# Optimization experiments

Hardware: AMD Instinct MI355X
Metric: run time of the kernel (lower is better)

Reference implementation:

```python
import jax, jax.numpy as jnp
import numpy as np

N_NODES = 100000
N_EDGES = 1600000
IN_F = 67
H1, C1 = 10, 8   # heads, per-head channels layer 1
H2, C2 = 1, 1    # layer 2


def setup_inputs() -> dict:
    key = jax.random.key(0)
    ks = jax.random.split(key, 10)
    x = jax.random.normal(ks[0], (N_NODES, IN_F), dtype=jnp.float32)
    edge_index = jax.random.randint(ks[1], (2, N_EDGES), 0, N_NODES, dtype=jnp.int64)
    s = 0.1
    W1 = jax.random.normal(ks[2], (IN_F, H1 * C1), dtype=jnp.float32) * s
    att_src1 = jax.random.normal(ks[3], (H1, C1), dtype=jnp.float32) * s
    att_dst1 = jax.random.normal(ks[4], (H1, C1), dtype=jnp.float32) * s
    b1 = jnp.zeros((H1 * C1,), dtype=jnp.float32)
    W2 = jax.random.normal(ks[5], (H1 * C1, H2 * C2), dtype=jnp.float32) * s
    att_src2 = jax.random.normal(ks[6], (H2, C2), dtype=jnp.float32) * s
    att_dst2 = jax.random.normal(ks[7], (H2, C2), dtype=jnp.float32) * s
    b2 = jnp.zeros((H2 * C2,), dtype=jnp.float32)
    return {"x": x, "edge_index": edge_index, "W1": W1, "att_src1": att_src1,
            "att_dst1": att_dst1, "b1": b1, "W2": W2, "att_src2": att_src2,
            "att_dst2": att_dst2, "b2": b2}


def gat_conv(x, src, dst, W, att_src, att_dst, bias, heads, out_ch):
    """PyG GATConv (eval mode): gather -> leaky_relu -> segment softmax -> scatter."""
    n = x.shape[0]
    h = (x @ W).reshape(n, heads, out_ch)                     # [N,H,C]
    a_src = jnp.sum(h * att_src, axis=-1)                     # [N,H]
    a_dst = jnp.sum(h * att_dst, axis=-1)                     # [N,H]
    e = a_src[src] + a_dst[dst]                               # [E,H]
    e = jax.nn.leaky_relu(e, negative_slope=0.2)
    # numerically stable softmax over edges grouped by destination node
    m = jax.ops.segment_max(e, dst, num_segments=n)           # [N,H]
    ex = jnp.exp(e - m[dst])
    denom = jax.ops.segment_sum(ex, dst, num_segments=n)      # [N,H]
    alpha = ex / denom[dst]                                   # [E,H]
    msg = h[src] * alpha[:, :, None]                          # [E,H,C]
    out = jax.ops.segment_sum(msg, dst, num_segments=n)       # [N,H,C]
    return out.reshape(n, heads * out_ch) + bias


def reference(x, edge_index, W1, att_src1, att_dst1, b1, W2, att_src2, att_dst2, b2):
    n = x.shape[0]
    loops = jnp.arange(n, dtype=edge_index.dtype)
    src = jnp.concatenate([edge_index[0], loops])             # add_self_loops=True
    dst = jnp.concatenate([edge_index[1], loops])
    h = gat_conv(x, src, dst, W1, att_src1, att_dst1, b1, H1, C1)
    h = jax.nn.elu(h)
    out = gat_conv(h, src, dst, W2, att_src2, att_dst2, b2, H2, C2)
    return out
```

## Files before the change

### kernel.cpp

```cpp
#include <hip/hip_runtime.h>
#include <math.h>

#define IN_F 67
#define F1   80
#define NH1  10
#define NC1  8

#define GN   64
#define KS   104
#define PKS  96

#define CB    512
#define CSH   9
#define NBC   196
#define RB    64
#define NGRP  8
#define GCAP  1536
#define SLCAP 1664
#define CSTRIDE 16
#define NFB   782
#define CHUNK 2048
#define A2T   4

typedef _Float16 h16;
typedef h16 h16x2 __attribute__((ext_vector_type(2)));
typedef h16 h16x8 __attribute__((ext_vector_type(8)));
typedef float f32x4 __attribute__((ext_vector_type(4)));
typedef float f32x4u __attribute__((ext_vector_type(4), aligned(4)));
typedef int i32x4 __attribute__((ext_vector_type(4)));

__global__ __launch_bounds__(256)
void k_front(const float* __restrict__ x, const float* __restrict__ W,
             const float* __restrict__ att_s, const float* __restrict__ att_d,
             const int* __restrict__ ei, int* __restrict__ gcur,
             int* __restrict__ ebuf, h16* __restrict__ pk,
             float* __restrict__ a_dst, int N, int E) {
    __shared__ __align__(16) char smem[GN * 81 * 4];
    const int tid = threadIdx.x;

    if ((int)blockIdx.x < NFB) {
        int2* sStage = (int2*)smem;
        int*  sCnt   = (int*)(smem + CHUNK * 8);
        int*  sGBase = sCnt + NBC;
        int*  sScan  = sGBase + NBC;
        int*  wsum   = sScan + 256;
        const int g = blockIdx.x & (NGRP - 1);
        const int lane = tid & 63;
        const int wv = tid >> 6;

        int base_e = blockIdx.x * CHUNK;
        if (base_e < E) {
            int lim = E - base_e; if (lim > CHUNK) lim = CHUNK;
            for (int i = tid; i < NBC; i += 256) sCnt[i] = 0;
            __syncthreads();

            int2 ev[8]; int pos[8]; int nloc = 0;
            int e0 = base_e + tid * 8;
            if (tid * 8 + 8 <= lim) {
                i32x4 s0 = *(const i32x4*)(ei + e0);
                i32x4 s1 = *(const i32x4*)(ei + e0 + 4);
                i32x4 d0 = *(const i32x4*)(ei + E + e0);
                i32x4 d1 = *(const i32x4*)(ei + E + e0 + 4);
#pragma unroll
                for (int j = 0; j < 4; ++j) { ev[j] = make_int2(s0[j], d0[j]); }
#pragma unroll
                for (int j = 0; j < 4; ++j) { ev[4 + j] = make_int2(s1[j], d1[j]); }
                nloc = 8;
            } else {
                for (int j = 0; j < 8; ++j) {
                    int e = e0 + j;
                    if (tid * 8 + j < lim) { ev[nloc++] = make_int2(ei[e], ei[E + e]); }
                }
            }
            for (int j = 0; j < nloc; ++j)
                pos[j] = atomicAdd(&sCnt[ev[j].y >> CSH], 1);
            __syncthreads();

            int v = (tid < NBC) ? sCnt[tid] : 0;
            int sc = v;
#pragma unroll
            for (int o = 1; o < 64; o <<= 1) {
                int u = __shfl_up(sc, o);
                if (lane >= o) sc += u;
            }
            if (lane == 63) wsum[wv] = sc;
            __syncthreads();
            int add = 0;
#pragma unroll
            for (int w = 0; w < 4; ++w) add += (w < wv) ? wsum[w] : 0;
            sScan[tid] = sc + add;
            if (tid < NBC && v > 0)
                sGBase[tid] = atomicAdd(&gcur[((size_t)g * NBC + tid) * CSTRIDE], v);
            __syncthreads();

            for (int j = 0; j < nloc; ++j) {
                int B = ev[j].y >> CSH;
                sStage[sScan[B] - sCnt[B] + pos[j]] = ev[j];
            }
            __syncthreads();

            int total = sScan[NBC - 1];
            for (int i = tid; i < total; i += 256) {
                int2 e = sStage[i];
                int B = e.y >> CSH;
                int gp = sGBase[B] + (i - (sScan[B] - sCnt[B]));
                if (gp < GCAP)
                    ebuf[((size_t)g * NBC + B) * GCAP + gp] = e.x | ((e.y & (CB - 1)) << 17);
            }
        }
        return;
    }

    h16*   sWt = (h16*)smem;
    float* sO  = (float*)smem;
    const int node0 = (blockIdx.x - NFB) * GN;

    for (int idx = tid; idx < F1 * 96; idx += 256) {
        int k = idx / F1;
        int c = idx - k * F1;
        sWt[c * KS + k] = (h16)(k < IN_F ? W[idx] : 0.f);
    }
    __syncthreads();

    const int lane = tid & 63;
    const int m    = lane & 15;
    const int quad = lane >> 4;
    const int wn0  = (tid >> 6) * 16;

    int gn  = node0 + wn0 + m;
    int gnc = gn < N ? gn : N - 1;
    const float* xr = x + (size_t)gnc * IN_F;

    f32x4 acc[5];
#pragma unroll
    for (int ct = 0; ct < 5; ++ct) acc[ct] = (f32x4){0.f, 0.f, 0.f, 0.f};

#pragma unroll
    for (int ks = 0; ks < 64; ks += 32) {
        int k0 = ks + quad * 8;
        f32x4 a0 = *(const f32x4u*)(xr + k0);
        f32x4 a1 = *(const f32x4u*)(xr + k0 + 4);
        h16x8 af;
        af[0] = (h16)a0.x; af[1] = (h16)a0.y; af[2] = (h16)a0.z; af[3] = (h16)a0.w;
        af[4] = (h16)a1.x; af[5] = (h16)a1.y; af[6] = (h16)a1.z; af[7] = (h16)a1.w;
#pragma unroll
        for (int ct = 0; ct < 5; ++ct) {
            h16x8 bf = *(const h16x8*)(sWt + (ct * 16 + m) * KS + ks + quad * 8);
            acc[ct] = __builtin_amdgcn_mfma_f32_16x16x32_f16(af, bf, acc[ct], 0, 0, 0);
        }
    }
    {
        h16x8 af = (h16x8)(h16)0.f;
        if (quad == 0) {
            af[0] = (h16)xr[64]; af[1] = (h16)xr[65]; af[2] = (h16)xr[66];
        }
#pragma unroll
        for (int ct = 0; ct < 5; ++ct) {
            h16x8 bf = *(const h16x8*)(sWt + (ct * 16 + m) * KS + 64 + quad * 8);
            acc[ct] = __builtin_amdgcn_mfma_f32_16x16x32_f16(af, bf, acc[ct], 0, 0, 0);
        }
    }
    __syncthreads();

#pragma unroll
    for (int ct = 0; ct < 5; ++ct)
#pragma unroll
        for (int r = 0; r < 4; ++r)
            sO[(wn0 + quad * 4 + r) * 81 + ct * 16 + m] = acc[ct][r];
    __syncthreads();

    for (int idx = tid; idx < GN * (F1 / 2); idx += 256) {
        int n = idx / (F1 / 2);
        int p = idx - n * (F1 / 2);
        int gg = node0 + n;
        if (gg < N) {
            h16x2 v;
            v.x = (h16)sO[n * 81 + 2 * p];
            v.y = (h16)sO[n * 81 + 2 * p + 1];
            *(h16x2*)(pk + (size_t)gg * PKS + 2 * p) = v;
        }
    }
    for (int t = tid; t < GN * NH1; t += 256) {
        int n = t / NH1;
        int h = t - n * NH1;
        int gg = node0 + n;
        if (gg < N) {
            const float* hr = sO + n * 81 + h * NC1;
            float s = 0.f, d = 0.f;
#pragma unroll
            for (int c = 0; c < NC1; ++c) {
                float v = hr[c];
                s += v * att_s[h * NC1 + c];
                d += v * att_d[h * NC1 + c];
            }
            pk[(size_t)gg * PKS + F1 + h] = (h16)s;
            a_dst[gg * NH1 + h] = d;
        }
    }
}

__global__ __launch_bounds__(256)
void k_agg1(const int* __restrict__ ebuf, const int* __restrict__ gcur,
            const h16* __restrict__ pk, const float* __restrict__ a_dst,
            const float* __restrict__ b1, const float* __restrict__ W2,
            float* __restrict__ hl2acc,
            int* __restrict__ row, int* __restrict__ deg, int* __restrict__ csr2,
            int N, int NB) {
    __shared__ int   sTmp[SLCAP];
    __shared__ int   sList[SLCAP];
    __shared__ int   s_cnt[RB];
    __shared__ int   s_scan[RB];
    __shared__ int   s_cur[RB];
    __shared__ float s_acc[RB];
    __shared__ int   sTot;

    const int tid = threadIdx.x;
    const int lane = tid & 63;
    const int b = blockIdx.x;
    const int B = b >> 3;
    const int q = b & 7;
    const int lo = b * RB;

    for (int i = tid; i < RB; i += 256) { s_cnt[i] = 1; s_acc[i] = 0.f; }
    if (tid == 0) sTot = 0;
    __syncthreads();

    for (int g = 0; g < NGRP; ++g) {
        size_t slot = (size_t)g * NBC + B;
        int cnt = gcur[slot * CSTRIDE];
        cnt = cnt < GCAP ? cnt : GCAP;
        const int* eb = ebuf + slot * GCAP;
        for (int i0 = 0; i0 < cnt; i0 += 256) {
            int i = i0 + tid;
            int v = 0, n_l = 0;
            bool match = false;
            if (i < cnt) {
                v = eb[i];
                int dloc = v >> 17;
                match = (dloc >> 6) == q;
                n_l = dloc & (RB - 1);
            }
            unsigned long long mk = __ballot(match);
            int base = 0;
            if (lane == 0 && mk) base = atomicAdd(&sTot, __popcll(mk));
            base = __shfl(base, 0);
            if (match) {
                atomicAdd(&s_cnt[n_l], 1);
                int p = base + __popcll(mk & ((1ull << lane) - 1));
                if (p < SLCAP) sTmp[p] = (v & 0x1FFFF) | (n_l << 17);
            }
        }
    }
    __syncthreads();

    if (tid < RB) {
        int cntv = s_cnt[tid];
        int sc = cntv;
#pragma unroll
        for (int o = 1; o < RB; o <<= 1) {
            int u = __shfl_up(sc, o);
            if (tid >= o) sc += u;
        }
        s_scan[tid] = sc;
        int excl = sc - cntv;
        int n = lo + tid;
        if (excl < SLCAP) sList[excl] = n;
        s_cur[tid] = excl + 1;
        if (n < N) {
            int dg = cntv;
            if (excl + dg > SLCAP) dg = SLCAP - excl > 0 ? SLCAP - excl : 0;
            row[n] = b * SLCAP + excl;
            deg[n] = dg;
        }
    }
    __syncthreads();

    int total = sTot < SLCAP ? sTot : SLCAP;
    for (int i = tid; i < total; i += 256) {
        int u = sTmp[i];
        int n_l = u >> 17;
        int p = atomicAdd(&s_cur[n_l], 1);
        if (p < SLCAP) sList[p] = u & 0x1FFFF;
    }
    __syncthreads();

    int tot2 = s_scan[RB - 1];
    tot2 = tot2 < SLCAP ? tot2 : SLCAP;
    for (int i = tid; i < tot2; i += 256)
        csr2[(size_t)b * SLCAP + i] = sList[i];

    for (int t = tid; t < RB * NH1; t += 256) {
        int n_l = t / NH1;
        int h = t - n_l * NH1;
        int n = lo + n_l;
        if (n >= N) continue;
        int beg = s_scan[n_l] - s_cnt[n_l];
        int end = beg + s_cnt[n_l];
        end = end < SLCAP ? end : SLCAP;
        float ad = a_dst[n * NH1 + h];
        float den = 0.f;
        float num[NC1];
#pragma unroll
        for (int c = 0; c < NC1; ++c) num[c] = 0.f;

        int i = beg;
        for (; i + 3 < end; i += 4) {
            int sv[4];
#pragma unroll
            for (int j = 0; j < 4; ++j) sv[j] = sList[i + j];
            h16x8 qf[4];
            float a[4];
#pragma unroll
            for (int j = 0; j < 4; ++j) {
                const h16* rp = pk + (size_t)sv[j] * PKS;
                qf[j] = *(const h16x8*)(rp + h * NC1);
                a[j] = (float)rp[F1 + h];
            }
#pragma unroll
            for (int j = 0; j < 4; ++j) {
                float v = a[j] + ad;
                v = v > 0.f ? v : 0.2f * v;
                float w = __expf(v);
                den += w;
#pragma unroll
                for (int c = 0; c < NC1; ++c) num[c] += w * (float)qf[j][c];
            }
        }
        for (; i < end; ++i) {
            const h16* rp = pk + (size_t)sList[i] * PKS;
            h16x8 qf = *(const h16x8*)(rp + h * NC1);
            float v = (float)rp[F1 + h] + ad;
            v = v > 0.f ? v : 0.2f * v;
            float w = __expf(v);
            den += w;
#pragma unroll
            for (int c = 0; c < NC1; ++c) num[c] += w * (float)qf[c];
        }
        float inv = 1.f / den;
        const float* bb = b1 + h * NC1;
        const float* w2 = W2 + h * NC1;
        float p = 0.f;
#pragma unroll
        for (int c = 0; c < NC1; ++c) {
            float o = num[c] * inv + bb[c];
            o = o > 0.f ? o : expm1f(o);
            p += o * w2[c];
        }
        atomicAdd(&s_acc[n_l], p);
    }
    __syncthreads();

    if (tid < RB) {
        int n = lo + tid;
        if (n < N) hl2acc[n] = s_acc[tid];
    }
}

__global__ __launch_bounds__(256)
void k_agg2(const int* __restrict__ row, const int* __restrict__ deg,
            const int* __restrict__ csr2, const float* __restrict__ hl2acc,
            const float* __restrict__ att_s2, const float* __restrict__ att_d2,
            const float* __restrict__ b2, float* __restrict__ out, int N) {
    int t = blockIdx.x * blockDim.x + threadIdx.x;
    int n = t >> 2;
    int sl = t & (A2T - 1);
    if (n >= N) return;
    float as2 = att_s2[0];
    float ad = hl2acc[n] * att_d2[0];
    int beg = row[n];
    int dg  = deg[n];
    float den = 0.f, num = 0.f;
    int i = sl;
    for (; i + A2T < dg; i += 2 * A2T) {
        int s0 = csr2[beg + i];
        int s1 = csr2[beg + i + A2T];
        float g0 = hl2acc[s0];
        float g1 = hl2acc[s1];
        float v0 = g0 * as2 + ad; v0 = v0 > 0.f ? v0 : 0.2f * v0;
        float v1 = g1 * as2 + ad; v1 = v1 > 0.f ? v1 : 0.2f * v1;
        float w0 = __expf(v0), w1 = __expf(v1);
        den += w0 + w1;
        num += w0 * g0 + w1 * g1;
    }
    for (; i < dg; i += A2T) {
        float g = hl2acc[csr2[beg + i]];
        float v = g * as2 + ad;
        v = v > 0.f ? v : 0.2f * v;
        float w = __expf(v);
        den += w;
        num += w * g;
    }
    den += __shfl_xor(den, 1); num += __shfl_xor(num, 1);
    den += __shfl_xor(den, 2); num += __shfl_xor(num, 2);
    if (sl == 0) out[n] = num / den + b2[0];
}

extern "C" void kernel_launch(void* const* d_in, const int* in_sizes, int n_in,
                              void* d_out, int out_size, void* d_ws, size_t ws_size,
                              hipStream_t stream) {
    const float* x        = (const float*)d_in[0];
    const int*   ei       = (const int*)d_in[1];
    const float* W1       = (const float*)d_in[2];
    const float* att_src1 = (const float*)d_in[3];
    const float* att_dst1 = (const float*)d_in[4];
    const float* b1       = (const float*)d_in[5];
    const float* W2       = (const float*)d_in[6];
    const float* att_src2 = (const float*)d_in[7];
    const float* att_dst2 = (const float*)d_in[8];
    const float* b2       = (const float*)d_in[9];
    float* out = (float*)d_out;

    const int N  = in_sizes[0] / IN_F;
    const int E  = in_sizes[1] / 2;
    const int NB = (N + RB - 1) / RB;

    float*  ws      = (float*)d_ws;
    h16*    pk      = (h16*)ws;
    float*  a_dst1  = ws + (size_t)N * (PKS / 2);
    float*  hl2acc  = a_dst1 + (size_t)N * NH1;
    int*    row     = (int*)(hl2acc + N);
    int*    deg     = row + N;
    int*    gcur    = deg + N;
    int*    csr2    = gcur + (size_t)NGRP * NBC * CSTRIDE;
    int*    ebuf    = csr2 + (size_t)NB * SLCAP;

    const int B = 256;
    const int nbG = (N + GN - 1) / GN;

    hipMemsetAsync(gcur, 0, (size_t)NGRP * NBC * CSTRIDE * sizeof(int), stream);
    k_front<<<NFB + nbG, 256, 0, stream>>>(x, W1, att_src1, att_dst1, ei,
                                           gcur, ebuf, pk, a_dst1, N, E);

    k_agg1<<<NB, 256, 0, stream>>>(ebuf, gcur, pk, a_dst1, b1, W2,
                                   hl2acc, row, deg, csr2, N, NB);

    k_agg2<<<((size_t)N * A2T + B - 1) / B, B, 0, stream>>>(row, deg, csr2, hl2acc,
                                                            att_src2, att_dst2, b2,
                                                            out, N);
}
```

Before: 216.4 us.

## Split fused front kernel and interleave per-head features with attention scores

Splits the combined edge-bucketing/GEMM kernel into two separate launches. It also changes the packed node row layout so that each head's 8 fp16 features sit next to that head's source attention score (10 halfs per head, row stride 100). The gather in the aggregation kernel then touches one contiguous 20-byte span per edge instead of two separate locations. The cost is unaligned vector loads (4-byte alignment), an extra kernel launch, and losing the overlap of fill and GEMM work within a single grid.

```diff
diff --git a/kernel.cpp b/kernel.cpp
--- a/kernel.cpp
+++ b/kernel.cpp
@@ -8,7 +8,7 @@
 
 #define GN   64
 #define KS   104
-#define PKS  96
+#define PKS  100
 
 #define CB    512
 #define CSH   9
@@ -25,95 +25,95 @@
 typedef _Float16 h16;
 typedef h16 h16x2 __attribute__((ext_vector_type(2)));
 typedef h16 h16x8 __attribute__((ext_vector_type(8)));
+typedef h16 h16x8u __attribute__((ext_vector_type(8), aligned(4)));
 typedef float f32x4 __attribute__((ext_vector_type(4)));
 typedef float f32x4u __attribute__((ext_vector_type(4), aligned(4)));
 typedef int i32x4 __attribute__((ext_vector_type(4)));
 
 __global__ __launch_bounds__(256)
-void k_front(const float* __restrict__ x, const float* __restrict__ W,
-             const float* __restrict__ att_s, const float* __restrict__ att_d,
-             const int* __restrict__ ei, int* __restrict__ gcur,
-             int* __restrict__ ebuf, h16* __restrict__ pk,
-             float* __restrict__ a_dst, int N, int E) {
+void k_fill(const int* __restrict__ ei, int* __restrict__ gcur,
+            int* __restrict__ ebuf, int E) {
+    __shared__ __align__(16) char smem[CHUNK * 8 + NBC * 8 + 256 * 4 + 16];
+    int2* sStage = (int2*)smem;
+    int*  sCnt   = (int*)(smem + CHUNK * 8);
+    int*  sGBase = sCnt + NBC;
+    int*  sScan  = sGBase + NBC;
+    int*  wsum   = sScan + 256;
+    const int tid = threadIdx.x;
+    const int g = blockIdx.x & (NGRP - 1);
+    const int lane = tid & 63;
+    const int wv = tid >> 6;
+
+    int base_e = blockIdx.x * CHUNK;
+    if (base_e >= E) return;
+    int lim = E - base_e; if (lim > CHUNK) lim = CHUNK;
+    for (int i = tid; i < NBC; i += 256) sCnt[i] = 0;
+    __syncthreads();
+
+    int2 ev[8]; int pos[8]; int nloc = 0;
+    int e0 = base_e + tid * 8;
+    if (tid * 8 + 8 <= lim) {
+        i32x4 s0 = *(const i32x4*)(ei + e0);
+        i32x4 s1 = *(const i32x4*)(ei + e0 + 4);
+        i32x4 d0 = *(const i32x4*)(ei + E + e0);
+        i32x4 d1 = *(const i32x4*)(ei + E + e0 + 4);
+#pragma unroll
+        for (int j = 0; j < 4; ++j) { ev[j] = make_int2(s0[j], d0[j]); }
+#pragma unroll
+        for (int j = 0; j < 4; ++j) { ev[4 + j] = make_int2(s1[j], d1[j]); }
+        nloc = 8;
+    } else {
+        for (int j = 0; j < 8; ++j) {
+            int e = e0 + j;
+            if (tid * 8 + j < lim) { ev[nloc++] = make_int2(ei[e], ei[E + e]); }
+        }
+    }
+    for (int j = 0; j < nloc; ++j)
+        pos[j] = atomicAdd(&sCnt[ev[j].y >> CSH], 1);
+    __syncthreads();
+
+    int v = (tid < NBC) ? sCnt[tid] : 0;
+    int sc = v;
+#pragma unroll
+    for (int o = 1; o < 64; o <<= 1) {
+        int u = __shfl_up(sc, o);
+        if (lane >= o) sc += u;
+    }
+    if (lane == 63) wsum[wv] = sc;
+    __syncthreads();
+    int add = 0;
+#pragma unroll
+    for (int w = 0; w < 4; ++w) add += (w < wv) ? wsum[w] : 0;
+    sScan[tid] = sc + add;
+    if (tid < NBC && v > 0)
+        sGBase[tid] = atomicAdd(&gcur[((size_t)g * NBC + tid) * CSTRIDE], v);
+    __syncthreads();
+
+    for (int j = 0; j < nloc; ++j) {
+        int B = ev[j].y >> CSH;
+        sStage[sScan[B] - sCnt[B] + pos[j]] = ev[j];
+    }
+    __syncthreads();
+
+    int total = sScan[NBC - 1];
+    for (int i = tid; i < total; i += 256) {
+        int2 e = sStage[i];
+        int B = e.y >> CSH;
+        int gp = sGBase[B] + (i - (sScan[B] - sCnt[B]));
+        if (gp < GCAP)
+            ebuf[((size_t)g * NBC + B) * GCAP + gp] = e.x | ((e.y & (CB - 1)) << 17);
+    }
+}
+
+__global__ __launch_bounds__(256)
+void k_gemm(const float* __restrict__ x, const float* __restrict__ W,
+            const float* __restrict__ att_s, const float* __restrict__ att_d,
+            h16* __restrict__ pk, float* __restrict__ a_dst, int N) {
     __shared__ __align__(16) char smem[GN * 81 * 4];
-    const int tid = threadIdx.x;
-
-    if ((int)blockIdx.x < NFB) {
-        int2* sStage = (int2*)smem;
-        int*  sCnt   = (int*)(smem + CHUNK * 8);
-        int*  sGBase = sCnt + NBC;
-        int*  sScan  = sGBase + NBC;
-        int*  wsum   = sScan + 256;
-        const int g = blockIdx.x & (NGRP - 1);
-        const int lane = tid & 63;
-        const int wv = tid >> 6;
-
-        int base_e = blockIdx.x * CHUNK;
-        if (base_e < E) {
-            int lim = E - base_e; if (lim > CHUNK) lim = CHUNK;
-            for (int i = tid; i < NBC; i += 256) sCnt[i] = 0;
-            __syncthreads();
-
-            int2 ev[8]; int pos[8]; int nloc = 0;
-            int e0 = base_e + tid * 8;
-            if (tid * 8 + 8 <= lim) {
-                i32x4 s0 = *(const i32x4*)(ei + e0);
-                i32x4 s1 = *(const i32x4*)(ei + e0 + 4);
-                i32x4 d0 = *(const i32x4*)(ei + E + e0);
-                i32x4 d1 = *(const i32x4*)(ei + E + e0 + 4);
-#pragma unroll
-                for (int j = 0; j < 4; ++j) { ev[j] = make_int2(s0[j], d0[j]); }
-#pragma unroll
-                for (int j = 0; j < 4; ++j) { ev[4 + j] = make_int2(s1[j], d1[j]); }
-                nloc = 8;
-            } else {
-                for (int j = 0; j < 8; ++j) {
-                    int e = e0 + j;
-                    if (tid * 8 + j < lim) { ev[nloc++] = make_int2(ei[e], ei[E + e]); }
-                }
-            }
-            for (int j = 0; j < nloc; ++j)
-                pos[j] = atomicAdd(&sCnt[ev[j].y >> CSH], 1);
-            __syncthreads();
-
-            int v = (tid < NBC) ? sCnt[tid] : 0;
-            int sc = v;
-#pragma unroll
-            for (int o = 1; o < 64; o <<= 1) {
-                int u = __shfl_up(sc, o);
-                if (lane >= o) sc += u;
-            }
-            if (lane == 63) wsum[wv] = sc;
-            __syncthreads();
-            int add = 0;
-#pragma unroll
-            for (int w = 0; w < 4; ++w) add += (w < wv) ? wsum[w] : 0;
-            sScan[tid] = sc + add;
-            if (tid < NBC && v > 0)
-                sGBase[tid] = atomicAdd(&gcur[((size_t)g * NBC + tid) * CSTRIDE], v);
-            __syncthreads();
-
-            for (int j = 0; j < nloc; ++j) {
-                int B = ev[j].y >> CSH;
-                sStage[sScan[B] - sCnt[B] + pos[j]] = ev[j];
-            }
-            __syncthreads();
-
-            int total = sScan[NBC - 1];
-            for (int i = tid; i < total; i += 256) {
-                int2 e = sStage[i];
-                int B = e.y >> CSH;
-                int gp = sGBase[B] + (i - (sScan[B] - sCnt[B]));
-                if (gp < GCAP)
-                    ebuf[((size_t)g * NBC + B) * GCAP + gp] = e.x | ((e.y & (CB - 1)) << 17);
-            }
-        }
-        return;
-    }
-
     h16*   sWt = (h16*)smem;
     float* sO  = (float*)smem;
-    const int node0 = (blockIdx.x - NFB) * GN;
+    const int tid = threadIdx.x;
+    const int node0 = blockIdx.x * GN;
 
     for (int idx = tid; idx < F1 * 96; idx += 256) {
         int k = idx / F1;
@@ -169,31 +169,24 @@
             sO[(wn0 + quad * 4 + r) * 81 + ct * 16 + m] = acc[ct][r];
     __syncthreads();
 
-    for (int idx = tid; idx < GN * (F1 / 2); idx += 256) {
-        int n = idx / (F1 / 2);
-        int p = idx - n * (F1 / 2);
-        int gg = node0 + n;
-        if (gg < N) {
-            h16x2 v;
-            v.x = (h16)sO[n * 81 + 2 * p];
-            v.y = (h16)sO[n * 81 + 2 * p + 1];
-            *(h16x2*)(pk + (size_t)gg * PKS + 2 * p) = v;
-        }
-    }
     for (int t = tid; t < GN * NH1; t += 256) {
         int n = t / NH1;
         int h = t - n * NH1;
         int gg = node0 + n;
         if (gg < N) {
             const float* hr = sO + n * 81 + h * NC1;
+            h16x8 vf;
             float s = 0.f, d = 0.f;
 #pragma unroll
             for (int c = 0; c < NC1; ++c) {
                 float v = hr[c];
+                vf[c] = (h16)v;
                 s += v * att_s[h * NC1 + c];
                 d += v * att_d[h * NC1 + c];
             }
-            pk[(size_t)gg * PKS + F1 + h] = (h16)s;
+            h16* slot = pk + (size_t)gg * PKS + h * 10;
+            *(h16x8u*)slot = vf;
+            slot[8] = (h16)s;
             a_dst[gg * NH1 + h] = d;
         }
     }
@@ -312,9 +305,9 @@
             float a[4];
 #pragma unroll
             for (int j = 0; j < 4; ++j) {
-                const h16* rp = pk + (size_t)sv[j] * PKS;
-                qf[j] = *(const h16x8*)(rp + h * NC1);
-                a[j] = (float)rp[F1 + h];
+                const h16* rp = pk + (size_t)sv[j] * PKS + h * 10;
+                qf[j] = *(const h16x8u*)rp;
+                a[j] = (float)rp[8];
             }
 #pragma unroll
             for (int j = 0; j < 4; ++j) {
@@ -327,9 +320,9 @@
             }
         }
         for (; i < end; ++i) {
-            const h16* rp = pk + (size_t)sList[i] * PKS;
-            h16x8 qf = *(const h16x8*)(rp + h * NC1);
-            float v = (float)rp[F1 + h] + ad;
+            const h16* rp = pk + (size_t)sList[i] * PKS + h * 10;
+            h16x8 qf = *(const h16x8u*)rp;
+            float v = (float)rp[8] + ad;
             v = v > 0.f ? v : 0.2f * v;
             float w = __expf(v);
             den += w;
@@ -428,12 +421,10 @@
     const int nbG = (N + GN - 1) / GN;
 
     hipMemsetAsync(gcur, 0, (size_t)NGRP * NBC * CSTRIDE * sizeof(int), stream);
-    k_front<<<NFB + nbG, 256, 0, stream>>>(x, W1, att_src1, att_dst1, ei,
-                                           gcur, ebuf, pk, a_dst1, N, E);
-
+    k_fill<<<NFB, 256, 0, stream>>>(ei, gcur, ebuf, E);
+    k_gemm<<<nbG, 256, 0, stream>>>(x, W1, att_src1, att_dst1, pk, a_dst1, N);
     k_agg1<<<NB, 256, 0, stream>>>(ebuf, gcur, pk, a_dst1, b1, W2,
                                    hl2acc, row, deg, csr2, N, NB);
-
     k_agg2<<<((size_t)N * A2T + B - 1) / B, B, 0, stream>>>(row, deg, csr2, hl2acc,
                                                             att_src2, att_dst2, b2,
                                                             out, N);
```

Measured after the change: 241.4 us. 1.12x slower.

## Add sub-bucket split pass so agg1 reads only its own edges

Applied to the files above, without the earlier changes.

Splits the fused front kernel into separate edge-fill and GEMM kernels. It adds a k_split pass that regroups each coarse destination bucket into 8 fine sub-buckets (capped at FCAP entries each). Before, each of the 8 agg1 blocks sharing a bucket scanned the whole bucket and filtered it with ballots. Now each block reads only its own contiguous sub-list, with no shared-memory atomic counter. The cost is an extra launch and one more edge pass, losing the overlap between fill and GEMM work, and csr2 now aliases the ebuf workspace.

```diff
diff --git a/kernel.cpp b/kernel.cpp
--- a/kernel.cpp
+++ b/kernel.cpp
@@ -16,6 +16,7 @@
 #define RB    64
 #define NGRP  8
 #define GCAP  1536
+#define FCAP  320
 #define SLCAP 1664
 #define CSTRIDE 16
 #define NFB   782
@@ -30,90 +31,135 @@
 typedef int i32x4 __attribute__((ext_vector_type(4)));
 
 __global__ __launch_bounds__(256)
-void k_front(const float* __restrict__ x, const float* __restrict__ W,
-             const float* __restrict__ att_s, const float* __restrict__ att_d,
-             const int* __restrict__ ei, int* __restrict__ gcur,
-             int* __restrict__ ebuf, h16* __restrict__ pk,
-             float* __restrict__ a_dst, int N, int E) {
+void k_fill(const int* __restrict__ ei, int* __restrict__ gcur,
+            int* __restrict__ ebuf, int E) {
+    __shared__ __align__(16) char smem[CHUNK * 8 + NBC * 8 + 256 * 4 + 16];
+    int2* sStage = (int2*)smem;
+    int*  sCnt   = (int*)(smem + CHUNK * 8);
+    int*  sGBase = sCnt + NBC;
+    int*  sScan  = sGBase + NBC;
+    int*  wsum   = sScan + 256;
+    const int tid = threadIdx.x;
+    const int g = blockIdx.x & (NGRP - 1);
+    const int lane = tid & 63;
+    const int wv = tid >> 6;
+
+    int base_e = blockIdx.x * CHUNK;
+    if (base_e >= E) return;
+    int lim = E - base_e; if (lim > CHUNK) lim = CHUNK;
+    for (int i = tid; i < NBC; i += 256) sCnt[i] = 0;
+    __syncthreads();
+
+    int2 ev[8]; int pos[8]; int nloc = 0;
+    int e0 = base_e + tid * 8;
+    if (tid * 8 + 8 <= lim) {
+        i32x4 s0 = *(const i32x4*)(ei + e0);
+        i32x4 s1 = *(const i32x4*)(ei + e0 + 4);
+        i32x4 d0 = *(const i32x4*)(ei + E + e0);
+        i32x4 d1 = *(const i32x4*)(ei + E + e0 + 4);
+#pragma unroll
+        for (int j = 0; j < 4; ++j) { ev[j] = make_int2(s0[j], d0[j]); }
+#pragma unroll
+        for (int j = 0; j < 4; ++j) { ev[4 + j] = make_int2(s1[j], d1[j]); }
+        nloc = 8;
+    } else {
+        for (int j = 0; j < 8; ++j) {
+            int e = e0 + j;
+            if (tid * 8 + j < lim) { ev[nloc++] = make_int2(ei[e], ei[E + e]); }
+        }
+    }
+    for (int j = 0; j < nloc; ++j)
+        pos[j] = atomicAdd(&sCnt[ev[j].y >> CSH], 1);
+    __syncthreads();
+
+    int v = (tid < NBC) ? sCnt[tid] : 0;
+    int sc = v;
+#pragma unroll
+    for (int o = 1; o < 64; o <<= 1) {
+        int u = __shfl_up(sc, o);
+        if (lane >= o) sc += u;
+    }
+    if (lane == 63) wsum[wv] = sc;
+    __syncthreads();
+    int add = 0;
+#pragma unroll
+    for (int w = 0; w < 4; ++w) add += (w < wv) ? wsum[w] : 0;
+    sScan[tid] = sc + add;
+    if (tid < NBC && v > 0)
+        sGBase[tid] = atomicAdd(&gcur[((size_t)g * NBC + tid) * CSTRIDE], v);
+    __syncthreads();
+
+    for (int j = 0; j < nloc; ++j) {
+        int B = ev[j].y >> CSH;
+        sStage[sScan[B] - sCnt[B] + pos[j]] = ev[j];
+    }
+    __syncthreads();
+
+    int total = sScan[NBC - 1];
+    for (int i = tid; i < total; i += 256) {
+        int2 e = sStage[i];
+        int B = e.y >> CSH;
+        int gp = sGBase[B] + (i - (sScan[B] - sCnt[B]));
+        if (gp < GCAP)
+            ebuf[((size_t)g * NBC + B) * GCAP + gp] = e.x | ((e.y & (CB - 1)) << 17);
+    }
+}
+
+__global__ __launch_bounds__(256)
+void k_split(const int* __restrict__ ebuf, const int* __restrict__ gcur,
+             int* __restrict__ ebuf2, int* __restrict__ fcnt) {
+    __shared__ int sE[GCAP];
+    __shared__ int sE2[GCAP];
+    __shared__ int cnt8[8], off8[8], cur8[8];
+    const int tid = threadIdx.x;
+    const int slot = blockIdx.x;
+    int cnt = gcur[(size_t)slot * CSTRIDE];
+    cnt = cnt < GCAP ? cnt : GCAP;
+    const int* eb = ebuf + (size_t)slot * GCAP;
+
+    if (tid < 8) cnt8[tid] = 0;
+    __syncthreads();
+    for (int i = tid; i < cnt; i += 256) {
+        int v = eb[i];
+        sE[i] = v;
+        atomicAdd(&cnt8[(v >> 23) & 7], 1);
+    }
+    __syncthreads();
+    if (tid == 0) {
+        int o = 0;
+#pragma unroll
+        for (int f = 0; f < 8; ++f) { off8[f] = o; cur8[f] = o; o += cnt8[f]; }
+    }
+    __syncthreads();
+    for (int i = tid; i < cnt; i += 256) {
+        int v = sE[i];
+        int p = atomicAdd(&cur8[(v >> 23) & 7], 1);
+        sE2[p] = v;
+    }
+    __syncthreads();
+    for (int i = tid; i < cnt; i += 256) {
+        int f = 0;
+#pragma unroll
+        for (int k = 1; k < 8; ++k) f += (i >= off8[k]);
+        int idx = i - off8[f];
+        if (idx < FCAP)
+            ebuf2[((size_t)slot * 8 + f) * FCAP + idx] = sE2[i];
+    }
+    if (tid < 8) {
+        int c = cnt8[tid];
+        fcnt[slot * 8 + tid] = c < FCAP ? c : FCAP;
+    }
+}
+
+__global__ __launch_bounds__(256)
+void k_gemm(const float* __restrict__ x, const float* __restrict__ W,
+            const float* __restrict__ att_s, const float* __restrict__ att_d,
+            h16* __restrict__ pk, float* __restrict__ a_dst, int N) {
     __shared__ __align__(16) char smem[GN * 81 * 4];
-    const int tid = threadIdx.x;
-
-    if ((int)blockIdx.x < NFB) {
-        int2* sStage = (int2*)smem;
-        int*  sCnt   = (int*)(smem + CHUNK * 8);
-        int*  sGBase = sCnt + NBC;
-        int*  sScan  = sGBase + NBC;
-        int*  wsum   = sScan + 256;
-        const int g = blockIdx.x & (NGRP - 1);
-        const int lane = tid & 63;
-        const int wv = tid >> 6;
-
-        int base_e = blockIdx.x * CHUNK;
-        if (base_e < E) {
-            int lim = E - base_e; if (lim > CHUNK) lim = CHUNK;
-            for (int i = tid; i < NBC; i += 256) sCnt[i] = 0;
-            __syncthreads();
-
-            int2 ev[8]; int pos[8]; int nloc = 0;
-            int e0 = base_e + tid * 8;
-            if (tid * 8 + 8 <= lim) {
-                i32x4 s0 = *(const i32x4*)(ei + e0);
-                i32x4 s1 = *(const i32x4*)(ei + e0 + 4);
-                i32x4 d0 = *(const i32x4*)(ei + E + e0);
-                i32x4 d1 = *(const i32x4*)(ei + E + e0 + 4);
-#pragma unroll
-                for (int j = 0; j < 4; ++j) { ev[j] = make_int2(s0[j], d0[j]); }
-#pragma unroll
-                for (int j = 0; j < 4; ++j) { ev[4 + j] = make_int2(s1[j], d1[j]); }
-                nloc = 8;
-            } else {
-                for (int j = 0; j < 8; ++j) {
-                    int e = e0 + j;
-                    if (tid * 8 + j < lim) { ev[nloc++] = make_int2(ei[e], ei[E + e]); }
-                }
-            }
-            for (int j = 0; j < nloc; ++j)
-                pos[j] = atomicAdd(&sCnt[ev[j].y >> CSH], 1);
-            __syncthreads();
-
-            int v = (tid < NBC) ? sCnt[tid] : 0;
-            int sc = v;
-#pragma unroll
-            for (int o = 1; o < 64; o <<= 1) {
-                int u = __shfl_up(sc, o);
-                if (lane >= o) sc += u;
-            }
-            if (lane == 63) wsum[wv] = sc;
-            __syncthreads();
-            int add = 0;
-#pragma unroll
-            for (int w = 0; w < 4; ++w) add += (w < wv) ? wsum[w] : 0;
-            sScan[tid] = sc + add;
-            if (tid < NBC && v > 0)
-                sGBase[tid] = atomicAdd(&gcur[((size_t)g * NBC + tid) * CSTRIDE], v);
-            __syncthreads();
-
-            for (int j = 0; j < nloc; ++j) {
-                int B = ev[j].y >> CSH;
-                sStage[sScan[B] - sCnt[B] + pos[j]] = ev[j];
-            }
-            __syncthreads();
-
-            int total = sScan[NBC - 1];
-            for (int i = tid; i < total; i += 256) {
-                int2 e = sStage[i];
-                int B = e.y >> CSH;
-                int gp = sGBase[B] + (i - (sScan[B] - sCnt[B]));
-                if (gp < GCAP)
-                    ebuf[((size_t)g * NBC + B) * GCAP + gp] = e.x | ((e.y & (CB - 1)) << 17);
-            }
-        }
-        return;
-    }
-
     h16*   sWt = (h16*)smem;
     float* sO  = (float*)smem;
-    const int node0 = (blockIdx.x - NFB) * GN;
+    const int tid = threadIdx.x;
+    const int node0 = blockIdx.x * GN;
 
     for (int idx = tid; idx < F1 * 96; idx += 256) {
         int k = idx / F1;
@@ -200,7 +246,7 @@
 }
 
 __global__ __launch_bounds__(256)
-void k_agg1(const int* __restrict__ ebuf, const int* __restrict__ gcur,
+void k_agg1(const int* __restrict__ ebuf2, const int* __restrict__ fcnt,
             const h16* __restrict__ pk, const float* __restrict__ a_dst,
             const float* __restrict__ b1, const float* __restrict__ W2,
             float* __restrict__ hl2acc,
@@ -212,44 +258,29 @@
     __shared__ int   s_scan[RB];
     __shared__ int   s_cur[RB];
     __shared__ float s_acc[RB];
-    __shared__ int   sTot;
 
     const int tid = threadIdx.x;
-    const int lane = tid & 63;
     const int b = blockIdx.x;
     const int B = b >> 3;
     const int q = b & 7;
     const int lo = b * RB;
 
     for (int i = tid; i < RB; i += 256) { s_cnt[i] = 1; s_acc[i] = 0.f; }
-    if (tid == 0) sTot = 0;
-    __syncthreads();
-
+    __syncthreads();
+
+    int off = 0;
     for (int g = 0; g < NGRP; ++g) {
-        size_t slot = (size_t)g * NBC + B;
-        int cnt = gcur[slot * CSTRIDE];
-        cnt = cnt < GCAP ? cnt : GCAP;
-        const int* eb = ebuf + slot * GCAP;
-        for (int i0 = 0; i0 < cnt; i0 += 256) {
-            int i = i0 + tid;
-            int v = 0, n_l = 0;
-            bool match = false;
-            if (i < cnt) {
-                v = eb[i];
-                int dloc = v >> 17;
-                match = (dloc >> 6) == q;
-                n_l = dloc & (RB - 1);
-            }
-            unsigned long long mk = __ballot(match);
-            int base = 0;
-            if (lane == 0 && mk) base = atomicAdd(&sTot, __popcll(mk));
-            base = __shfl(base, 0);
-            if (match) {
-                atomicAdd(&s_cnt[n_l], 1);
-                int p = base + __popcll(mk & ((1ull << lane) - 1));
-                if (p < SLCAP) sTmp[p] = (v & 0x1FFFF) | (n_l << 17);
-            }
-        }
+        int slot2 = (g * NBC + B) * 8 + q;
+        int cnt = fcnt[slot2];
+        const int* eb = ebuf2 + (size_t)slot2 * FCAP;
+        for (int i = tid; i < cnt; i += 256) {
+            int v = eb[i];
+            int n_l = (v >> 17) & (RB - 1);
+            atomicAdd(&s_cnt[n_l], 1);
+            int p = off + i;
+            if (p < SLCAP) sTmp[p] = (v & 0x1FFFF) | (n_l << 17);
+        }
+        off += cnt;
     }
     __syncthreads();
 
@@ -275,7 +306,7 @@
     }
     __syncthreads();
 
-    int total = sTot < SLCAP ? sTot : SLCAP;
+    int total = off < SLCAP ? off : SLCAP;
     for (int i = tid; i < total; i += 256) {
         int u = sTmp[i];
         int n_l = u >> 17;
@@ -421,19 +452,20 @@
     int*    row     = (int*)(hl2acc + N);
     int*    deg     = row + N;
     int*    gcur    = deg + N;
-    int*    csr2    = gcur + (size_t)NGRP * NBC * CSTRIDE;
-    int*    ebuf    = csr2 + (size_t)NB * SLCAP;
+    int*    fcnt    = gcur + (size_t)NGRP * NBC * CSTRIDE;
+    int*    ebuf2   = fcnt + (size_t)NGRP * NBC * 8;
+    int*    ebuf    = ebuf2 + (size_t)NGRP * NBC * 8 * FCAP;
+    int*    csr2    = ebuf;
 
     const int B = 256;
     const int nbG = (N + GN - 1) / GN;
 
     hipMemsetAsync(gcur, 0, (size_t)NGRP * NBC * CSTRIDE * sizeof(int), stream);
-    k_front<<<NFB + nbG, 256, 0, stream>>>(x, W1, att_src1, att_dst1, ei,
-                                           gcur, ebuf, pk, a_dst1, N, E);
-
-    k_agg1<<<NB, 256, 0, stream>>>(ebuf, gcur, pk, a_dst1, b1, W2,
+    k_fill<<<NFB, 256, 0, stream>>>(ei, gcur, ebuf, E);
+    k_split<<<NGRP * NBC, 256, 0, stream>>>(ebuf, gcur, ebuf2, fcnt);
+    k_gemm<<<nbG, 256, 0, stream>>>(x, W1, att_src1, att_dst1, pk, a_dst1, N);
+    k_agg1<<<NB, 256, 0, stream>>>(ebuf2, fcnt, pk, a_dst1, b1, W2,
                                    hl2acc, row, deg, csr2, N, NB);
-
     k_agg2<<<((size_t)N * A2T + B - 1) / B, B, 0, stream>>>(row, deg, csr2, hl2acc,
                                                             att_src2, att_dst2, b2,
                                                             out, N);
```

Result: slower. 223.4 us (+3.2%).
